# Kernel tuning notes

Measured on AMD Instinct MI355X. Metric: run time of the kernel, lower is better.

Reference implementation:

```python
import jax, jax.numpy as jnp
import numpy as np

N_FEATURES = 170
D_MODEL = 64
N_HEADS = 4
ALPHA = 0.1
LN_EPS = 1e-5
LEAKY_SLOPE = 0.01  # torch F.leaky_relu default
N = 3 * N_FEATURES  # 510
B = 32


def setup_inputs() -> dict:
    key = jax.random.key(0)
    ks = jax.random.split(key, 10)
    D, H = D_MODEL, N_HEADS
    s = 1.0 / np.sqrt(D)
    return {
        "x": jax.random.normal(ks[0], (B, N, D), dtype=jnp.float32),
        "causal_graph": jax.random.uniform(ks[1], (N, N), dtype=jnp.float32),
        # nn.Linear(d_model, d_model*n_heads, bias=False): stored here as (D, H*D) for x @ W
        "W": jax.random.uniform(ks[2], (D, H * D), jnp.float32, -s, s),
        "attention_w": jax.random.normal(ks[3], (H, 2 * D), dtype=jnp.float32),
        # Conv2d(2, n_heads, 3, padding=1): OIHW kernel
        "conv_w": jax.random.uniform(ks[4], (H, 2, 3, 3), jnp.float32, -1/np.sqrt(18), 1/np.sqrt(18)),
        "conv_b": jax.random.uniform(ks[5], (H,), jnp.float32, -1/np.sqrt(18), 1/np.sqrt(18)),
        # nn.Linear(d_model, 2*d_model): stored as (D, 2D)
        "fcg_w": jax.random.uniform(ks[6], (D, 2 * D), jnp.float32, -s, s),
        "fcg_b": jax.random.uniform(ks[7], (2 * D,), jnp.float32, -s, s),
        "ln_g": jnp.ones((D,), jnp.float32),
        "ln_b": jnp.zeros((D,), jnp.float32),
    }


def reference(x, causal_graph, W, attention_w, conv_w, conv_b, fcg_w, fcg_b, ln_g, ln_b):
    Bz, Nn, D = x.shape
    H = N_HEADS
    # shared projection: (B, N, H, D)
    xt = (x @ W).reshape(Bz, Nn, H, D)
    # GAT-style additive scores: concat-dot decomposed into two dot products
    w1, w2 = attention_w[:, :D], attention_w[:, D:]  # each (H, D)
    s_i = jnp.einsum('bnhd,hd->bhn', xt, w1)  # source term
    s_j = jnp.einsum('bnhd,hd->bhn', xt, w2)  # target term
    e = s_i[:, :, :, None] + s_j[:, :, None, :]  # (B, H, N, N)
    A_eva = jnp.where(e >= 0, e, LEAKY_SLOPE * e)  # leaky_relu
    # fuse mean attention with causal graph via 3x3 conv
    A_mean = A_eva.mean(axis=1)  # (B, N, N)
    causal = jnp.broadcast_to(causal_graph[None], (Bz, Nn, Nn))
    stacked = jnp.stack([A_mean, causal], axis=1)  # (B, 2, N, N)
    A_st = jax.lax.conv_general_dilated(
        stacked, conv_w, window_strides=(1, 1), padding=((1, 1), (1, 1)),
        dimension_numbers=('NCHW', 'OIHW', 'NCHW'))
    A_st = A_st + conv_b[None, :, None, None]  # (B, H, N, N)
    A = jax.nn.softmax(ALPHA * A_eva + (1.0 - ALPHA) * A_st, axis=-1)
    # multi-head aggregation then head-mean
    out = jnp.einsum('bhnm,bmhd->bnhd', A, xt).mean(axis=2)  # (B, N, D)
    # GLU
    g = out @ fcg_w + fcg_b  # (B, N, 2D)
    a, b = g[..., :D], g[..., D:]
    glu = a * jax.nn.sigmoid(b)
    # residual + layernorm
    y = glu + x
    mu = y.mean(axis=-1, keepdims=True)
    var = ((y - mu) ** 2).mean(axis=-1, keepdims=True)
    y = (y - mu) * jax.lax.rsqrt(var + LN_EPS) * ln_g + ln_b
    return y, A
```

## Files before the change

### kernel.cpp

```cpp
#include <hip/hip_runtime.h>

#define Bz 32
#define Nn 510
#define Dd 64
#define Hh 4
#define HD_ 256
#define Kpad 512
#define ALPHA_ 0.1f
#define LNEPS 1e-5f
#define SLOPE 0.01f
#define NEG_INF -3.0e38f

typedef __attribute__((ext_vector_type(8))) short short8;
typedef __attribute__((ext_vector_type(4))) float floatx4;

__device__ inline float wredsum(float v) {
  #pragma unroll
  for (int off = 32; off; off >>= 1) v += __shfl_xor(v, off, 64);
  return v;
}
__device__ inline float wredmax(float v) {
  #pragma unroll
  for (int off = 32; off; off >>= 1) v = fmaxf(v, __shfl_xor(v, off, 64));
  return v;
}
__device__ inline unsigned short f2bf(float f) {
  unsigned int u = __float_as_uint(f);
  unsigned int r = (u + 0x7fffu + ((u >> 16) & 1u)) >> 16;
  return (unsigned short)r;
}

__global__ __launch_bounds__(256) void k1_xt(const float* __restrict__ x,
                                             const float* __restrict__ W,
                                             const float* __restrict__ attw,
                                             unsigned short* __restrict__ xtT,
                                             float* __restrict__ si,
                                             float* __restrict__ sj) {
  __shared__ float Wl[64][132];
  __shared__ float xr[32][68];
  const int t = threadIdx.x;
  const int rt = blockIdx.x;
  const int b = blockIdx.y;
  const int ch = blockIdx.z;
  #pragma unroll
  for (int k = 0; k < 8; k++) {
    int f = t + k * 256;
    int kr = f >> 5;
    int c = (f & 31) * 4;
    float4 v = *(const float4*)&W[kr * HD_ + ch * 128 + c];
    *(float4*)&Wl[kr][c] = v;
  }
  #pragma unroll
  for (int k = 0; k < 2; k++) {
    int f = t + k * 256;
    int r = f >> 4;
    int c = (f & 15) * 4;
    int row = rt * 32 + r;
    float4 v = make_float4(0.f, 0.f, 0.f, 0.f);
    if (row < Nn) v = *(const float4*)&x[(b * Nn + row) * Dd + c];
    *(float4*)&xr[r][c] = v;
  }
  __syncthreads();
  const int tr = t >> 5, tc = t & 31;
  const int rb = tr * 4, c0 = tc * 4;
  float acc[4][4] = {};
  #pragma unroll
  for (int k4 = 0; k4 < 16; k4++) {
    float4 xv[4];
    #pragma unroll
    for (int r = 0; r < 4; r++) xv[r] = *(float4*)&xr[rb + r][k4 * 4];
    #pragma unroll
    for (int kk = 0; kk < 4; kk++) {
      float4 wv = *(float4*)&Wl[k4 * 4 + kk][c0];
      #pragma unroll
      for (int r = 0; r < 4; r++) {
        float xs = (&xv[r].x)[kk];
        acc[r][0] = fmaf(xs, wv.x, acc[r][0]);
        acc[r][1] = fmaf(xs, wv.y, acc[r][1]);
        acc[r][2] = fmaf(xs, wv.z, acc[r][2]);
        acc[r][3] = fmaf(xs, wv.w, acc[r][3]);
      }
    }
  }
  const int colbase = ch * 128 + c0;
  const int h = colbase >> 6;
  const int dd = colbase & 63;
  const int m0r = rt * 32 + rb;
  #pragma unroll
  for (int cc = 0; cc < 4; cc++) {
    unsigned short* p = &xtT[((size_t)(b * 4 + h) * 64 + (dd + cc)) * Kpad + m0r];
    if (m0r + 3 < Nn) {
      ushort4 u;
      u.x = f2bf(acc[0][cc]); u.y = f2bf(acc[1][cc]);
      u.z = f2bf(acc[2][cc]); u.w = f2bf(acc[3][cc]);
      *(ushort4*)p = u;
    } else {
      #pragma unroll
      for (int r = 0; r < 4; r++) if (m0r + r < Nn) p[r] = f2bf(acc[r][cc]);
    }
  }
  float w1v[4], w2v[4];
  #pragma unroll
  for (int cc = 0; cc < 4; cc++) {
    w1v[cc] = attw[h * 128 + dd + cc];
    w2v[cc] = attw[h * 128 + 64 + dd + cc];
  }
  #pragma unroll
  for (int r = 0; r < 4; r++) {
    float p1 = acc[r][0] * w1v[0] + acc[r][1] * w1v[1] +
               acc[r][2] * w1v[2] + acc[r][3] * w1v[3];
    float p2 = acc[r][0] * w2v[0] + acc[r][1] * w2v[1] +
               acc[r][2] * w2v[2] + acc[r][3] * w2v[3];
    #pragma unroll
    for (int off = 1; off <= 8; off <<= 1) {
      p1 += __shfl_xor(p1, off, 64);
      p2 += __shfl_xor(p2, off, 64);
    }
    if ((tc & 15) == 0) {
      int row = m0r + r;
      if (row < Nn) {
        si[(b * 4 + h) * Nn + row] = p1;
        sj[(b * 4 + h) * Nn + row] = p2;
      }
    }
  }
}

__global__ __launch_bounds__(256) void k2_attn(const float* __restrict__ si,
                                               const float* __restrict__ sj,
                                               const float* __restrict__ causal,
                                               const float* __restrict__ convw,
                                               const float* __restrict__ convb,
                                               float* __restrict__ A) {
  __shared__ float am_t[10 * 8 * 68];
  __shared__ float cz_t[10 * 8 * 68];
  __shared__ float sjl[4 * 8 * 68];
  __shared__ float sil[4][12];
  const int t = threadIdx.x;
  const int i0 = blockIdx.x * 8;
  const int b = blockIdx.y;
  if (t < 40) {
    int h = t / 10, r = t % 10;
    int iq = i0 + r - 1;
    sil[h][r] = (iq >= 0 && iq < Nn) ? si[(b * 4 + h) * Nn + iq] : 0.f;
  }
  if (t >= 64 && t < 224) {
    int q = t - 64;
    int r = q >> 4, rem = q & 15;
    int e = rem >> 1, side = rem & 1;
    int idx = (r * 8 + e) * 68 + side * 65;
    am_t[idx] = 0.f;
    cz_t[idx] = 0.f;
  }
  for (int f = t; f < 2048; f += 256) {
    int h = f >> 9, j = f & 511;
    float v = (j < Nn) ? sj[(b * 4 + h) * Nn + j] : 0.f;
    sjl[(h * 8 + (j & 7)) * 68 + (j >> 3) + 1] = v;
  }
  __syncthreads();
  for (int f = t; f < 5120; f += 256) {
    int r = f >> 9, j = f & 511;
    int iq = i0 + r - 1;
    float am = 0.f, cz = 0.f;
    if (iq >= 0 && iq < Nn && j < Nn) {
      float s = 0.f;
      #pragma unroll
      for (int h = 0; h < 4; h++) {
        float e2 = sil[h][r] + sjl[(h * 8 + (j & 7)) * 68 + (j >> 3) + 1];
        s += (e2 >= 0.f) ? e2 : SLOPE * e2;
      }
      am = 0.25f * s;
      cz = causal[iq * Nn + j];
    }
    int idx = (r * 8 + (j & 7)) * 68 + (j >> 3) + 1;
    am_t[idx] = am;
    cz_t[idx] = cz;
  }
  __syncthreads();
  const int w = t >> 6, L = t & 63;
  const int j0 = L * 8;
  for (int pp = w; pp < 32; pp += 4) {
    const int il = pp >> 2, h = pp & 3;
    const int i = i0 + il;
    if (i >= Nn) continue;
    const int bh = b * 4 + h;
    const float sih = sil[h][il + 1];
    float cw[18];
    #pragma unroll
    for (int q = 0; q < 18; q++) cw[q] = convw[h * 18 + q];
    const float cb = convb[h];
    float conv[8];
    #pragma unroll
    for (int e = 0; e < 8; e++) conv[e] = cb;
    #pragma unroll
    for (int r3 = 0; r3 < 3; r3++) {
      const float* ba = &am_t[((il + r3) * 8) * 68];
      const float* bc = &cz_t[((il + r3) * 8) * 68];
      float a[10], c[10];
      a[0] = ba[7 * 68 + L];
      c[0] = bc[7 * 68 + L];
      #pragma unroll
      for (int e = 0; e < 8; e++) {
        a[1 + e] = ba[e * 68 + L + 1];
        c[1 + e] = bc[e * 68 + L + 1];
      }
      a[9] = ba[0 * 68 + L + 2];
      c[9] = bc[0 * 68 + L + 2];
      float w0 = cw[r3 * 3], w1 = cw[r3 * 3 + 1], w2 = cw[r3 * 3 + 2];
      float u0 = cw[9 + r3 * 3], u1 = cw[9 + r3 * 3 + 1], u2 = cw[9 + r3 * 3 + 2];
      #pragma unroll
      for (int e = 0; e < 8; e++) {
        float cv = conv[e];
        cv = fmaf(w0, a[e], cv);
        cv = fmaf(w1, a[e + 1], cv);
        cv = fmaf(w2, a[e + 2], cv);
        cv = fmaf(u0, c[e], cv);
        cv = fmaf(u1, c[e + 1], cv);
        cv = fmaf(u2, c[e + 2], cv);
        conv[e] = cv;
      }
    }
    float v[8];
    float mx = NEG_INF;
    #pragma unroll
    for (int e = 0; e < 8; e++) {
      float ee = sih + sjl[(h * 8 + e) * 68 + L + 1];
      float l = (ee >= 0.f) ? ee : SLOPE * ee;
      float val = ALPHA_ * l + (1.0f - ALPHA_) * conv[e];
      v[e] = (j0 + e < Nn) ? val : NEG_INF;
      mx = fmaxf(mx, v[e]);
    }
    mx = wredmax(mx);
    float p[8], s = 0.f;
    #pragma unroll
    for (int e = 0; e < 8; e++) {
      p[e] = __expf(v[e] - mx);
      s += p[e];
    }
    s = wredsum(s);
    const float inv = 1.f / s;
    #pragma unroll
    for (int e = 0; e < 8; e++) p[e] *= inv;
    float* Ar = &A[((size_t)bh * Nn + i) * Nn + j0];
    *(float4*)&Ar[0] = make_float4(p[0], p[1], p[2], p[3]);
    if (L < 63) {
      *(float4*)&Ar[4] = make_float4(p[4], p[5], p[6], p[7]);
    } else {
      *(float2*)&Ar[4] = make_float2(p[4], p[5]);
    }
  }
}

__global__ __launch_bounds__(256) void k3_out(const float* __restrict__ A,
                                              const unsigned short* __restrict__ xtT,
                                              const float* __restrict__ x,
                                              const float* __restrict__ fcgw,
                                              const float* __restrict__ fcgb,
                                              const float* __restrict__ lng,
                                              const float* __restrict__ lnb,
                                              float* __restrict__ y) {
  __shared__ unsigned short Asub[16 * 72];
  __shared__ unsigned short Xsub[64 * 72];
  __shared__ float ol[16][64];
  __shared__ float gl[2][128];
  const int t = threadIdx.x;
  const int n0 = blockIdx.x * 16;
  const int b = blockIdx.y;
  const int w = t >> 6, lane = t & 63;
  const int quad = lane >> 4, l16 = lane & 15;
  const int wc = w * 16;
  const int ar = t >> 4;
  const int amc = (t & 15) * 4;
  const int xd = t >> 2;
  const int xmc = (t & 3) * 16;
  floatx4 acc = {0.f, 0.f, 0.f, 0.f};
  for (int h = 0; h < 4; h++) {
    const float* Ab = &A[((size_t)(b * 4 + h) * Nn + n0) * Nn];
    const unsigned short* Xb = &xtT[(size_t)(b * 4 + h) * 64 * Kpad];
    for (int kt = 0; kt < 8; kt++) {
      const int m0 = kt * 64;
      __syncthreads();
      {
        int n = n0 + ar;
        int m = m0 + amc;
        float av[4] = {0.f, 0.f, 0.f, 0.f};
        if (n < Nn) {
          const float* src = &Ab[(size_t)ar * Nn + m];
          if (m + 3 < Nn) {
            *(float4*)av = *(const float4*)src;
          } else {
            int lim = Nn - m;
            #pragma unroll
            for (int q = 0; q < 4; q++) if (q < lim) av[q] = src[q];
          }
        }
        ushort4 u;
        u.x = f2bf(av[0]); u.y = f2bf(av[1]);
        u.z = f2bf(av[2]); u.w = f2bf(av[3]);
        *(ushort4*)&Asub[ar * 72 + amc] = u;
        const unsigned short* xs = &Xb[(size_t)xd * Kpad + m0 + xmc];
        short8 x0 = *(const short8*)&xs[0];
        short8 x1 = *(const short8*)&xs[8];
        *(short8*)&Xsub[xd * 72 + xmc] = x0;
        *(short8*)&Xsub[xd * 72 + xmc + 8] = x1;
      }
      __syncthreads();
      #pragma unroll
      for (int ks = 0; ks < 2; ks++) {
        short8 af = *(short8*)&Asub[l16 * 72 + ks * 32 + quad * 8];
        short8 bf = *(short8*)&Xsub[(wc + l16) * 72 + ks * 32 + quad * 8];
        acc = __builtin_amdgcn_mfma_f32_16x16x32_bf16(af, bf, acc, 0, 0, 0);
      }
    }
  }
  __syncthreads();
  #pragma unroll
  for (int reg = 0; reg < 4; reg++) {
    ol[quad * 4 + reg][wc + l16] = 0.25f * acc[reg];
  }
  __syncthreads();
  const int kk = t & 127;
  const int rg = t >> 7;
  for (int it = 0; it < 8; it++) {
    const int r = it * 2 + rg;
    const int row = n0 + r;
    float g = fcgb[kk];
    #pragma unroll
    for (int d = 0; d < 64; d++) g = fmaf(ol[r][d], fcgw[d * 128 + kk], g);
    gl[rg][kk] = g;
    __syncthreads();
    if (kk < 64 && row < Nn) {
      float a = gl[rg][kk];
      float bb = gl[rg][kk + 64];
      float glu = a / (1.f + __expf(-bb));
      float yv = glu + x[(b * Nn + row) * Dd + kk];
      float mu = wredsum(yv) * (1.f / 64.f);
      float dv = yv - mu;
      float var = wredsum(dv * dv) * (1.f / 64.f);
      float o = dv * rsqrtf(var + LNEPS) * lng[kk] + lnb[kk];
      y[(b * Nn + row) * Dd + kk] = o;
    }
    __syncthreads();
  }
}

extern "C" void kernel_launch(void* const* d_in, const int* in_sizes, int n_in,
                              void* d_out, int out_size, void* d_ws, size_t ws_size,
                              hipStream_t stream) {
  const float* x      = (const float*)d_in[0];
  const float* causal = (const float*)d_in[1];
  const float* W      = (const float*)d_in[2];
  const float* attw   = (const float*)d_in[3];
  const float* convw  = (const float*)d_in[4];
  const float* convb  = (const float*)d_in[5];
  const float* fcgw   = (const float*)d_in[6];
  const float* fcgb   = (const float*)d_in[7];
  const float* lng    = (const float*)d_in[8];
  const float* lnb    = (const float*)d_in[9];

  float* ws = (float*)d_ws;
  float* si = ws;
  float* sj = si + (size_t)Bz * Hh * Nn;
  unsigned short* xtT = (unsigned short*)(sj + (size_t)Bz * Hh * Nn + 16);
  size_t xtT_bytes = (size_t)Bz * Hh * Dd * Kpad * sizeof(unsigned short);

  float* yout = (float*)d_out;
  float* Aout = yout + (size_t)Bz * Nn * Dd;

  hipMemsetAsync(xtT, 0, xtT_bytes, stream);
  k1_xt <<<dim3(16, Bz, 2), 256, 0, stream>>>(x, W, attw, xtT, si, sj);
  k2_attn<<<dim3(64, Bz), 256, 0, stream>>>(si, sj, causal, convw, convb, Aout);
  k3_out <<<dim3(32, Bz), 256, 0, stream>>>(Aout, xtT, x, fcgw, fcgb, lng, lnb, yout);
}
```

Measured before the change: 308.0 us.

## Stage k1 output through LDS, drop memset, feed k3 MFMA directly from global

```diff
diff --git a/kernel.cpp b/kernel.cpp
--- a/kernel.cpp
+++ b/kernel.cpp
@@ -36,19 +36,19 @@
                                              unsigned short* __restrict__ xtT,
                                              float* __restrict__ si,
                                              float* __restrict__ sj) {
-  __shared__ float Wl[64][132];
+  __shared__ float Wl[64][68];
   __shared__ float xr[32][68];
+  __shared__ unsigned short st[64 * 33];
   const int t = threadIdx.x;
   const int rt = blockIdx.x;
   const int b = blockIdx.y;
   const int ch = blockIdx.z;
   #pragma unroll
-  for (int k = 0; k < 8; k++) {
+  for (int k = 0; k < 4; k++) {
     int f = t + k * 256;
-    int kr = f >> 5;
-    int c = (f & 31) * 4;
-    float4 v = *(const float4*)&W[kr * HD_ + ch * 128 + c];
-    *(float4*)&Wl[kr][c] = v;
+    int kr = f >> 4;
+    int c = (f & 15) * 4;
+    *(float4*)&Wl[kr][c] = *(const float4*)&W[kr * HD_ + ch * 64 + c];
   }
   #pragma unroll
   for (int k = 0; k < 2; k++) {
@@ -61,52 +61,44 @@
     *(float4*)&xr[r][c] = v;
   }
   __syncthreads();
-  const int tr = t >> 5, tc = t & 31;
-  const int rb = tr * 4, c0 = tc * 4;
-  float acc[4][4] = {};
+  const int tg = t >> 4;
+  const int tc = t & 15;
+  const int rb = tg * 2, c0 = tc * 4;
+  float acc[2][4] = {};
   #pragma unroll
   for (int k4 = 0; k4 < 16; k4++) {
-    float4 xv[4];
-    #pragma unroll
-    for (int r = 0; r < 4; r++) xv[r] = *(float4*)&xr[rb + r][k4 * 4];
+    float4 xv0 = *(float4*)&xr[rb][k4 * 4];
+    float4 xv1 = *(float4*)&xr[rb + 1][k4 * 4];
     #pragma unroll
     for (int kk = 0; kk < 4; kk++) {
       float4 wv = *(float4*)&Wl[k4 * 4 + kk][c0];
-      #pragma unroll
-      for (int r = 0; r < 4; r++) {
-        float xs = (&xv[r].x)[kk];
-        acc[r][0] = fmaf(xs, wv.x, acc[r][0]);
-        acc[r][1] = fmaf(xs, wv.y, acc[r][1]);
-        acc[r][2] = fmaf(xs, wv.z, acc[r][2]);
-        acc[r][3] = fmaf(xs, wv.w, acc[r][3]);
-      }
-    }
-  }
-  const int colbase = ch * 128 + c0;
-  const int h = colbase >> 6;
-  const int dd = colbase & 63;
-  const int m0r = rt * 32 + rb;
+      float xs0 = (&xv0.x)[kk];
+      float xs1 = (&xv1.x)[kk];
+      acc[0][0] = fmaf(xs0, wv.x, acc[0][0]);
+      acc[0][1] = fmaf(xs0, wv.y, acc[0][1]);
+      acc[0][2] = fmaf(xs0, wv.z, acc[0][2]);
+      acc[0][3] = fmaf(xs0, wv.w, acc[0][3]);
+      acc[1][0] = fmaf(xs1, wv.x, acc[1][0]);
+      acc[1][1] = fmaf(xs1, wv.y, acc[1][1]);
+      acc[1][2] = fmaf(xs1, wv.z, acc[1][2]);
+      acc[1][3] = fmaf(xs1, wv.w, acc[1][3]);
+    }
+  }
   #pragma unroll
   for (int cc = 0; cc < 4; cc++) {
-    unsigned short* p = &xtT[((size_t)(b * 4 + h) * 64 + (dd + cc)) * Kpad + m0r];
-    if (m0r + 3 < Nn) {
-      ushort4 u;
-      u.x = f2bf(acc[0][cc]); u.y = f2bf(acc[1][cc]);
-      u.z = f2bf(acc[2][cc]); u.w = f2bf(acc[3][cc]);
-      *(ushort4*)p = u;
-    } else {
-      #pragma unroll
-      for (int r = 0; r < 4; r++) if (m0r + r < Nn) p[r] = f2bf(acc[r][cc]);
+    #pragma unroll
+    for (int r = 0; r < 2; r++) {
+      st[(c0 + cc) * 33 + rb + r] = f2bf(acc[r][cc]);
     }
   }
   float w1v[4], w2v[4];
   #pragma unroll
   for (int cc = 0; cc < 4; cc++) {
-    w1v[cc] = attw[h * 128 + dd + cc];
-    w2v[cc] = attw[h * 128 + 64 + dd + cc];
-  }
-  #pragma unroll
-  for (int r = 0; r < 4; r++) {
+    w1v[cc] = attw[ch * 128 + c0 + cc];
+    w2v[cc] = attw[ch * 128 + 64 + c0 + cc];
+  }
+  #pragma unroll
+  for (int r = 0; r < 2; r++) {
     float p1 = acc[r][0] * w1v[0] + acc[r][1] * w1v[1] +
                acc[r][2] * w1v[2] + acc[r][3] * w1v[3];
     float p2 = acc[r][0] * w2v[0] + acc[r][1] * w2v[1] +
@@ -116,12 +108,23 @@
       p1 += __shfl_xor(p1, off, 64);
       p2 += __shfl_xor(p2, off, 64);
     }
-    if ((tc & 15) == 0) {
-      int row = m0r + r;
+    if (tc == 0) {
+      int row = rt * 32 + rb + r;
       if (row < Nn) {
-        si[(b * 4 + h) * Nn + row] = p1;
-        sj[(b * 4 + h) * Nn + row] = p2;
-      }
+        si[(b * 4 + ch) * Nn + row] = p1;
+        sj[(b * 4 + ch) * Nn + row] = p2;
+      }
+    }
+  }
+  __syncthreads();
+  if (t < 64) {
+    unsigned short* dst = &xtT[((size_t)(b * 4 + ch) * 64 + t) * Kpad + rt * 32];
+    #pragma unroll
+    for (int q = 0; q < 4; q++) {
+      short8 v;
+      #pragma unroll
+      for (int k = 0; k < 8; k++) v[k] = (short)st[t * 33 + q * 8 + k];
+      *(short8*)&dst[q * 8] = v;
     }
   }
 }
@@ -259,61 +262,47 @@
                                               const float* __restrict__ lng,
                                               const float* __restrict__ lnb,
                                               float* __restrict__ y) {
-  __shared__ unsigned short Asub[16 * 72];
-  __shared__ unsigned short Xsub[64 * 72];
   __shared__ float ol[16][64];
   __shared__ float gl[2][128];
   const int t = threadIdx.x;
   const int n0 = blockIdx.x * 16;
   const int b = blockIdx.y;
-  const int w = t >> 6, lane = t & 63;
-  const int quad = lane >> 4, l16 = lane & 15;
+  const int w = t >> 6, L = t & 63;
+  const int quad = L >> 4, l16 = L & 15;
   const int wc = w * 16;
-  const int ar = t >> 4;
-  const int amc = (t & 15) * 4;
-  const int xd = t >> 2;
-  const int xmc = (t & 3) * 16;
+  const int arow = (n0 + l16 < Nn) ? (n0 + l16) : (Nn - 1);
   floatx4 acc = {0.f, 0.f, 0.f, 0.f};
   for (int h = 0; h < 4; h++) {
-    const float* Ab = &A[((size_t)(b * 4 + h) * Nn + n0) * Nn];
-    const unsigned short* Xb = &xtT[(size_t)(b * 4 + h) * 64 * Kpad];
-    for (int kt = 0; kt < 8; kt++) {
-      const int m0 = kt * 64;
-      __syncthreads();
-      {
-        int n = n0 + ar;
-        int m = m0 + amc;
-        float av[4] = {0.f, 0.f, 0.f, 0.f};
-        if (n < Nn) {
-          const float* src = &Ab[(size_t)ar * Nn + m];
-          if (m + 3 < Nn) {
-            *(float4*)av = *(const float4*)src;
-          } else {
-            int lim = Nn - m;
-            #pragma unroll
-            for (int q = 0; q < 4; q++) if (q < lim) av[q] = src[q];
-          }
+    const float* Ar = &A[((size_t)(b * 4 + h) * Nn + arow) * Nn];
+    const unsigned short* Xr = &xtT[((size_t)(b * 4 + h) * 64 + wc + l16) * Kpad];
+    #pragma unroll 4
+    for (int kt = 0; kt < 16; kt++) {
+      const int m = kt * 32 + quad * 8;
+      float av[8];
+      if (m != 504) {
+        #pragma unroll
+        for (int q = 0; q < 4; q++) {
+          float2 v = *(const float2*)&Ar[m + q * 2];
+          av[q * 2] = v.x;
+          av[q * 2 + 1] = v.y;
         }
-        ushort4 u;
-        u.x = f2bf(av[0]); u.y = f2bf(av[1]);
-        u.z = f2bf(av[2]); u.w = f2bf(av[3]);
-        *(ushort4*)&Asub[ar * 72 + amc] = u;
-        const unsigned short* xs = &Xb[(size_t)xd * Kpad + m0 + xmc];
-        short8 x0 = *(const short8*)&xs[0];
-        short8 x1 = *(const short8*)&xs[8];
-        *(short8*)&Xsub[xd * 72 + xmc] = x0;
-        *(short8*)&Xsub[xd * 72 + xmc + 8] = x1;
-      }
-      __syncthreads();
-      #pragma unroll
-      for (int ks = 0; ks < 2; ks++) {
-        short8 af = *(short8*)&Asub[l16 * 72 + ks * 32 + quad * 8];
-        short8 bf = *(short8*)&Xsub[(wc + l16) * 72 + ks * 32 + quad * 8];
-        acc = __builtin_amdgcn_mfma_f32_16x16x32_bf16(af, bf, acc, 0, 0, 0);
-      }
-    }
-  }
-  __syncthreads();
+      } else {
+        #pragma unroll
+        for (int q = 0; q < 3; q++) {
+          float2 v = *(const float2*)&Ar[m + q * 2];
+          av[q * 2] = v.x;
+          av[q * 2 + 1] = v.y;
+        }
+        av[6] = 0.f;
+        av[7] = 0.f;
+      }
+      short8 af;
+      #pragma unroll
+      for (int e = 0; e < 8; e++) af[e] = (short)f2bf(av[e]);
+      short8 bf = *(const short8*)&Xr[m];
+      acc = __builtin_amdgcn_mfma_f32_16x16x32_bf16(af, bf, acc, 0, 0, 0);
+    }
+  }
   #pragma unroll
   for (int reg = 0; reg < 4; reg++) {
     ol[quad * 4 + reg][wc + l16] = 0.25f * acc[reg];
@@ -362,13 +351,11 @@
   float* si = ws;
   float* sj = si + (size_t)Bz * Hh * Nn;
   unsigned short* xtT = (unsigned short*)(sj + (size_t)Bz * Hh * Nn + 16);
-  size_t xtT_bytes = (size_t)Bz * Hh * Dd * Kpad * sizeof(unsigned short);
 
   float* yout = (float*)d_out;
   float* Aout = yout + (size_t)Bz * Nn * Dd;
 
-  hipMemsetAsync(xtT, 0, xtT_bytes, stream);
-  k1_xt <<<dim3(16, Bz, 2), 256, 0, stream>>>(x, W, attw, xtT, si, sj);
+  k1_xt  <<<dim3(16, Bz, 4), 256, 0, stream>>>(x, W, attw, xtT, si, sj);
   k2_attn<<<dim3(64, Bz), 256, 0, stream>>>(si, sj, causal, convw, convb, Aout);
   k3_out <<<dim3(32, Bz), 256, 0, stream>>>(Aout, xtT, x, fcgw, fcgb, lng, lnb, yout);
 }
```

Result: faster. 293.1 us (-4.8%).
